# Performance work log

Measured on AMD Instinct MI355X. Metric: run time of the kernel, lower is better.

The kernel has to match this reference:

```python
import jax, jax.numpy as jnp
import numpy as np

B, S, H, F, E, TOP_K = 2, 1024, 2048, 1408, 8, 2
SHARED_F = 2 * F  # moe_intermediate_size * n_shared_experts


def setup_inputs() -> dict:
    key = jax.random.key(0)
    ks = jax.random.split(key, 8)
    s = 0.02  # init scale for weights
    return {
        "hidden_states": jax.random.normal(ks[0], (B, S, H), jnp.float32),
        "gate_weight": jax.random.normal(ks[1], (E, H), jnp.float32) * s,
        "gate_proj": jax.random.normal(ks[2], (E, H, F), jnp.float32) * s,
        "up_proj": jax.random.normal(ks[3], (E, H, F), jnp.float32) * s,
        "down_proj": jax.random.normal(ks[4], (E, F, H), jnp.float32) * s,
        "shared_gate": jax.random.normal(ks[5], (H, SHARED_F), jnp.float32) * s,
        "shared_up": jax.random.normal(ks[6], (H, SHARED_F), jnp.float32) * s,
        "shared_down": jax.random.normal(ks[7], (SHARED_F, H), jnp.float32) * s,
    }


def reference(hidden_states, gate_weight, gate_proj, up_proj, down_proj,
              shared_gate, shared_up, shared_down):
    orig_shape = hidden_states.shape
    x = hidden_states.reshape(-1, orig_shape[-1])  # [T, H]
    T = x.shape[0]

    # MoEGate: softmax scores, top-k routing (no renorm)
    scores = jax.nn.softmax(x @ gate_weight.T, axis=-1)  # [T, E]
    topk_w, topk_idx = jax.lax.top_k(scores, TOP_K)      # [T, K]
    # dense combine weights: zero except selected experts
    combine = jnp.zeros_like(scores).at[jnp.arange(T)[:, None], topk_idx].set(topk_w)  # [T, E]

    # FusedSigmaMLP on all experts (math equal to sort/pad/grouped-GEMM/scatter-add path)
    gate_h = jnp.einsum('td,edf->etf', x, gate_proj)     # [E, T, F]
    up_h = jnp.einsum('td,edf->etf', x, up_proj)          # [E, T, F]
    expert_out = jnp.einsum('etf,efd->etd', jax.nn.silu(gate_h) * up_h, down_proj)  # [E, T, H]
    y = jnp.einsum('etd,te->td', expert_out, combine)     # weighted combine

    # shared experts (SigmaMLP with intermediate = moe_intermediate * n_shared)
    shared = (jax.nn.silu(x @ shared_gate) * (x @ shared_up)) @ shared_down
    return (y + shared).reshape(orig_shape)
```

## Files before the change

kernel.cpp:

```cpp
#include <hip/hip_runtime.h>
#include <hip/hip_bf16.h>

constexpr int T_ = 2048;
constexpr int H_ = 2048;
constexpr int F_ = 1408;
constexpr int E_ = 8;
constexpr int SF_ = 2816;

typedef __bf16 bf16;
typedef bf16 bf16x4 __attribute__((ext_vector_type(4)));
typedef bf16 bf16x8 __attribute__((ext_vector_type(8)));
typedef float f32x4 __attribute__((ext_vector_type(4)));

#define DEVI __device__ __forceinline__

constexpr int TR_GRID = 5280;
constexpr int PREP_GRID = TR_GRID + T_;
constexpr int GU_SH = 768;
constexpr int GU_EX = 3072;
constexpr int GU_GRID = GU_SH + GU_EX;
constexpr int DNSH_GRID = 512;
constexpr int DNEX_GRID = 2048;

DEVI void async16(const void* g, void* l) {
    __builtin_amdgcn_global_load_lds(
        (const __attribute__((address_space(1))) unsigned int*)g,
        (__attribute__((address_space(3))) unsigned int*)l, 16, 0, 0);
}

DEVI void transpose_tile(const float* __restrict__ src, bf16* __restrict__ dst,
                         int R, int C, int t, bf16* tile ) {
    int tiles_c = C >> 7;
    int r0 = (t / tiles_c) * 128, c0 = (t % tiles_c) * 128;
    int th = threadIdx.x;
    int fr = th >> 5;
    int fc = (th & 31) * 4;
#pragma unroll
    for (int p = 0; p < 16; p++) {
        int r = fr + p * 8;
        float4 v = *(const float4*)(src + (size_t)(r0 + r) * C + c0 + fc);
        bf16x4 b;
        b[0] = (bf16)v.x; b[1] = (bf16)v.y; b[2] = (bf16)v.z; b[3] = (bf16)v.w;
        *(bf16x4*)(tile + r * 132 + (fc ^ (r & 0x7C))) = b;
    }
    __syncthreads();
#pragma unroll
    for (int p = 0; p < 8; p++) {
        int ch = p * 256 + th;
        int c = ch >> 4, rq = ch & 15;
        bf16x8 o;
#pragma unroll
        for (int j = 0; j < 8; j++) {
            int row = rq * 8 + j;
            o[j] = tile[row * 132 + (c ^ (row & 0x7C))];
        }
        *(bf16x8*)(dst + (size_t)(c0 + c) * R + r0 + rq * 8) = o;
    }
}

DEVI void gate_route_token(const float* __restrict__ x, const float* __restrict__ gw,
                           bf16* __restrict__ xb, int* __restrict__ cnt,
                           int* __restrict__ list, float* __restrict__ wlist,
                           int t, float* wred ) {
    int tid = threadIdx.x;
    const float* xr = x + (size_t)t * H_;
    int h0 = tid * 8;
    float4 a = *(const float4*)(xr + h0);
    float4 b = *(const float4*)(xr + h0 + 4);
    float xv[8] = {a.x, a.y, a.z, a.w, b.x, b.y, b.z, b.w};
    bf16x8 v;
#pragma unroll
    for (int j = 0; j < 8; j++) v[j] = (bf16)xv[j];
    *(bf16x8*)(xb + (size_t)t * H_ + h0) = v;

    float p[E_];
#pragma unroll
    for (int e = 0; e < E_; e++) p[e] = 0.f;
#pragma unroll
    for (int j = 0; j < 8; j++)
#pragma unroll
        for (int e = 0; e < E_; e++) p[e] += xv[j] * gw[e * H_ + h0 + j];
#pragma unroll
    for (int e = 0; e < E_; e++)
#pragma unroll
        for (int off = 32; off > 0; off >>= 1) p[e] += __shfl_down(p[e], off, 64);
    int lane = tid & 63, wid = tid >> 6;
    if (lane == 0)
#pragma unroll
        for (int e = 0; e < E_; e++) wred[wid * E_ + e] = p[e];
    __syncthreads();
    if (tid == 0) {
        float l[E_];
#pragma unroll
        for (int e = 0; e < E_; e++)
            l[e] = wred[0 * E_ + e] + wred[1 * E_ + e] + wred[2 * E_ + e] + wred[3 * E_ + e];
        float mx = l[0];
#pragma unroll
        for (int e = 1; e < E_; e++) mx = fmaxf(mx, l[e]);
        float sc[E_], s = 0.f;
#pragma unroll
        for (int e = 0; e < E_; e++) { sc[e] = __expf(l[e] - mx); s += sc[e]; }
#pragma unroll
        for (int e = 0; e < E_; e++) sc[e] /= s;
        int i1 = 0;
#pragma unroll
        for (int e = 1; e < E_; e++) if (sc[e] > sc[i1]) i1 = e;
        int i2 = (i1 == 0) ? 1 : 0;
#pragma unroll
        for (int e = 0; e < E_; e++) if (e != i1 && sc[e] > sc[i2]) i2 = e;
        int p1 = atomicAdd(&cnt[i1], 1);
        list[i1 * T_ + p1] = t; wlist[i1 * T_ + p1] = sc[i1];
        int p2 = atomicAdd(&cnt[i2], 1);
        list[i2 * T_ + p2] = t; wlist[i2 * T_ + p2] = sc[i2];
    }
}

__global__ void fused_prep(const float* __restrict__ gp, const float* __restrict__ up,
                           const float* __restrict__ dp, const float* __restrict__ sg,
                           const float* __restrict__ su, const float* __restrict__ sd,
                           bf16* __restrict__ wg, bf16* __restrict__ wu,
                           bf16* __restrict__ wd, bf16* __restrict__ sgt,
                           bf16* __restrict__ sut, bf16* __restrict__ sdt,
                           const float* __restrict__ x, const float* __restrict__ gw,
                           bf16* __restrict__ xb, int* __restrict__ cnt,
                           int* __restrict__ list, float* __restrict__ wlist) {
    __shared__ __align__(16) bf16 tile[128 * 132];
    int id = blockIdx.x;
    if (id >= TR_GRID) {
        gate_route_token(x, gw, xb, cnt, list, wlist, id - TR_GRID, (float*)tile);
        return;
    }
    const float* src; bf16* dst; int R, C, t;
    if (id < 1408)      { int e = id / 176; t = id % 176; R = 2048; C = 1408;
                          src = gp + (size_t)e * R * C; dst = wg + (size_t)e * R * C; }
    else if (id < 2816) { int e = (id - 1408) / 176; t = (id - 1408) % 176; R = 2048; C = 1408;
                          src = up + (size_t)e * R * C; dst = wu + (size_t)e * R * C; }
    else if (id < 4224) { int e = (id - 2816) / 176; t = (id - 2816) % 176; R = 1408; C = 2048;
                          src = dp + (size_t)e * R * C; dst = wd + (size_t)e * R * C; }
    else if (id < 4576) { t = id - 4224; R = 2048; C = 2816; src = sg; dst = sgt; }
    else if (id < 4928) { t = id - 4576; R = 2048; C = 2816; src = su; dst = sut; }
    else                { t = id - 4928; R = 2816; C = 2048; src = sd; dst = sdt; }
    transpose_tile(src, dst, R, C, t, tile);
}

__global__ void gemm_gu(const bf16* __restrict__ xb,
                        const bf16* __restrict__ sgt, const bf16* __restrict__ sut,
                        const bf16* __restrict__ wg, const bf16* __restrict__ wu,
                        bf16* __restrict__ act_sh, bf16* __restrict__ act,
                        const int* __restrict__ cnt, const int* __restrict__ list,
                        const float* __restrict__ wlist) {
    int id = blockIdx.x;
    const bf16 *Bg, *Bu; bf16* C;
    const float* wl = nullptr;
    const int* lstA = nullptr;
    int M, N, row0, col0;
    if (id < GU_SH) {
        int x = id & 7, u = id >> 3;
        int cg = u >> 4, rb = u & 15;
        int col = cg * 8 + x;
        if (col >= 44) return;
        Bg = sgt; Bu = sut; C = act_sh;
        M = T_; N = SF_; row0 = rb * 128; col0 = col * 64;
    } else {
        int id2 = id - GU_SH;
        int x = id2 & 7, u = id2 >> 3;
        int e = u / 48, t2 = u % 48, j = t2 >> 4, rb = t2 & 15;
        int col = ((x - e) & 7) + 8 * j;
        if (col >= 22) return;
        M = cnt[e]; row0 = rb * 128;
        if (row0 >= M) return;
        lstA = list + (size_t)e * T_;
        Bg = wg + (size_t)e * F_ * H_;
        Bu = wu + (size_t)e * F_ * H_;
        C = act + (size_t)e * T_ * F_;
        wl = wlist + (size_t)e * T_;
        N = F_; col0 = col * 64;
    }

    __shared__ __align__(16) bf16 As[128 * 64];
    __shared__ __align__(16) bf16 Bgs[64 * 64];
    __shared__ __align__(16) bf16 Bus[64 * 64];

    int tid = threadIdx.x, lane = tid & 63, wid = tid >> 6;
    int wm = (wid >> 1) * 64, wn = (wid & 1) * 32;
    int lm = lane & 15, lq = lane >> 4;

    int srcrow[4];
#pragma unroll
    for (int j = 0; j < 4; j++) {
        int m = (j * 256 + tid) >> 3;
        int gr = row0 + m; if (gr >= M) gr = M - 1;
        srcrow[j] = lstA ? lstA[gr] : gr;
    }

    f32x4 accg[4][2] = {};
    f32x4 accu[4][2] = {};
    constexpr int nkt = H_ >> 6;

    for (int kt = 0; kt < nkt; kt++) {
        int k0 = kt * 64;
#pragma unroll
        for (int j = 0; j < 4; j++) {
            int L = j * 256 + tid;
            int m = L >> 3, cp = L & 7, c = cp ^ (m & 7);
            async16(xb + (size_t)srcrow[j] * H_ + k0 + c * 8, (void*)(As + L * 8));
        }
#pragma unroll
        for (int j = 0; j < 2; j++) {
            int L = j * 256 + tid;
            int n = L >> 3, cp = L & 7, c = cp ^ (n & 7);
            async16(Bg + (size_t)(col0 + n) * H_ + k0 + c * 8, (void*)(Bgs + L * 8));
            async16(Bu + (size_t)(col0 + n) * H_ + k0 + c * 8, (void*)(Bus + L * 8));
        }
        __syncthreads();
#pragma unroll
        for (int kk = 0; kk < 2; kk++) {
            bf16x8 af[4], bgf[2], buf_[2];
            int cc = kk * 4 + lq;
#pragma unroll
            for (int mi = 0; mi < 4; mi++) {
                int r = wm + mi * 16 + lm;
                af[mi] = *(const bf16x8*)(As + r * 64 + ((cc ^ (r & 7)) * 8));
            }
#pragma unroll
            for (int ni = 0; ni < 2; ni++) {
                int r = wn + ni * 16 + lm;
                bgf[ni]  = *(const bf16x8*)(Bgs + r * 64 + ((cc ^ (r & 7)) * 8));
                buf_[ni] = *(const bf16x8*)(Bus + r * 64 + ((cc ^ (r & 7)) * 8));
            }
#pragma unroll
            for (int mi = 0; mi < 4; mi++)
#pragma unroll
                for (int ni = 0; ni < 2; ni++) {
                    accg[mi][ni] = __builtin_amdgcn_mfma_f32_16x16x32_bf16(af[mi], bgf[ni], accg[mi][ni], 0, 0, 0);
                    accu[mi][ni] = __builtin_amdgcn_mfma_f32_16x16x32_bf16(af[mi], buf_[ni], accu[mi][ni], 0, 0, 0);
                }
        }
        __syncthreads();
    }
#pragma unroll
    for (int mi = 0; mi < 4; mi++)
#pragma unroll
        for (int r = 0; r < 4; r++) {
            int gr = row0 + wm + mi * 16 + lq * 4 + r;
            if (gr >= M) continue;
            float wv = wl ? wl[gr] : 1.f;
#pragma unroll
            for (int ni = 0; ni < 2; ni++) {
                int gc = col0 + wn + ni * 16 + lm;
                float g = accg[mi][ni][r], u = accu[mi][ni][r];
                float actv = wv * (g / (1.f + __expf(-g)) * u);
                C[(size_t)gr * N + gc] = (bf16)actv;
            }
        }
}

__global__ void gemm_down_sh(const bf16* __restrict__ act_sh, const bf16* __restrict__ sdt,
                             float* __restrict__ out) {
    int id = blockIdx.x;
    int x = id & 7, u = id >> 3;
    int cg = u >> 4, rb = u & 15;
    int col = cg * 8 + x;
    int row0 = rb * 128, col0 = col * 64;

    __shared__ __align__(16) bf16 As[128 * 64];
    __shared__ __align__(16) bf16 Bs[64 * 64];

    int tid = threadIdx.x, lane = tid & 63, wid = tid >> 6;
    int wm = (wid >> 1) * 64, wn = (wid & 1) * 32;
    int lm = lane & 15, lq = lane >> 4;

    f32x4 acc[4][2] = {};
    constexpr int nkt = SF_ >> 6;

    for (int kt = 0; kt < nkt; kt++) {
        int k0 = kt * 64;
#pragma unroll
        for (int j = 0; j < 4; j++) {
            int L = j * 256 + tid;
            int m = L >> 3, cp = L & 7, c = cp ^ (m & 7);
            async16(act_sh + (size_t)(row0 + m) * SF_ + k0 + c * 8, (void*)(As + L * 8));
        }
#pragma unroll
        for (int j = 0; j < 2; j++) {
            int L = j * 256 + tid;
            int n = L >> 3, cp = L & 7, c = cp ^ (n & 7);
            async16(sdt + (size_t)(col0 + n) * SF_ + k0 + c * 8, (void*)(Bs + L * 8));
        }
        __syncthreads();
#pragma unroll
        for (int kk = 0; kk < 2; kk++) {
            bf16x8 af[4], bfr[2];
            int cc = kk * 4 + lq;
#pragma unroll
            for (int i = 0; i < 4; i++) {
                int r = wm + i * 16 + lm;
                af[i] = *(const bf16x8*)(As + r * 64 + ((cc ^ (r & 7)) * 8));
            }
#pragma unroll
            for (int ni = 0; ni < 2; ni++) {
                int r = wn + ni * 16 + lm;
                bfr[ni] = *(const bf16x8*)(Bs + r * 64 + ((cc ^ (r & 7)) * 8));
            }
#pragma unroll
            for (int mi = 0; mi < 4; mi++)
#pragma unroll
                for (int ni = 0; ni < 2; ni++)
                    acc[mi][ni] = __builtin_amdgcn_mfma_f32_16x16x32_bf16(af[mi], bfr[ni], acc[mi][ni], 0, 0, 0);
        }
        __syncthreads();
    }
#pragma unroll
    for (int mi = 0; mi < 4; mi++)
#pragma unroll
        for (int r = 0; r < 4; r++) {
            int t = row0 + wm + mi * 16 + lq * 4 + r;
#pragma unroll
            for (int ni = 0; ni < 2; ni++) {
                int gc = col0 + wn + ni * 16 + lm;
                out[(size_t)t * H_ + gc] = acc[mi][ni][r];
            }
        }
}

__global__ void gemm_down_ex(const bf16* __restrict__ act, const bf16* __restrict__ wd,
                             float* __restrict__ out, const int* __restrict__ cnt,
                             const int* __restrict__ list) {
    int id = blockIdx.x;
    int x = id & 7, u = id >> 3;
    int e = u >> 5, t2 = u & 31, j = t2 >> 4, rb = t2 & 15;
    int col = ((x - e) & 7) + 8 * j;
    int M = cnt[e], row0 = rb * 128;
    if (row0 >= M) return;
    const bf16* A = act + (size_t)e * T_ * F_;
    const bf16* B = wd + (size_t)e * H_ * F_;
    const int* lst = list + (size_t)e * T_;
    int col0 = col * 128;

    __shared__ __align__(16) bf16 As[128 * 64];
    __shared__ __align__(16) bf16 Bs[128 * 64];

    int tid = threadIdx.x, lane = tid & 63, wid = tid >> 6;
    int wm = (wid >> 1) * 64, wn = (wid & 1) * 64;
    int lm = lane & 15, lq = lane >> 4;

    f32x4 acc[4][4] = {};
    constexpr int nkt = F_ >> 6;

    for (int kt = 0; kt < nkt; kt++) {
        int k0 = kt * 64;
#pragma unroll
        for (int j2 = 0; j2 < 4; j2++) {
            int L = j2 * 256 + tid;
            int m = L >> 3, cp = L & 7, c = cp ^ (m & 7);
            int gr = row0 + m; if (gr >= M) gr = M - 1;
            async16(A + (size_t)gr * F_ + k0 + c * 8, (void*)(As + L * 8));
            async16(B + (size_t)(col0 + m) * F_ + k0 + c * 8, (void*)(Bs + L * 8));
        }
        __syncthreads();
#pragma unroll
        for (int kk = 0; kk < 2; kk++) {
            bf16x8 af[4], bfr[4];
            int cc = kk * 4 + lq;
#pragma unroll
            for (int i = 0; i < 4; i++) {
                int ra = wm + i * 16 + lm;
                af[i] = *(const bf16x8*)(As + ra * 64 + ((cc ^ (ra & 7)) * 8));
                int rb2 = wn + i * 16 + lm;
                bfr[i] = *(const bf16x8*)(Bs + rb2 * 64 + ((cc ^ (rb2 & 7)) * 8));
            }
#pragma unroll
            for (int mi = 0; mi < 4; mi++)
#pragma unroll
                for (int ni = 0; ni < 4; ni++)
                    acc[mi][ni] = __builtin_amdgcn_mfma_f32_16x16x32_bf16(af[mi], bfr[ni], acc[mi][ni], 0, 0, 0);
        }
        __syncthreads();
    }
#pragma unroll
    for (int mi = 0; mi < 4; mi++)
#pragma unroll
        for (int r = 0; r < 4; r++) {
            int cr = row0 + wm + mi * 16 + lq * 4 + r;
            if (cr >= M) continue;
            int t = lst[cr];
#pragma unroll
            for (int ni = 0; ni < 4; ni++) {
                int gc = col0 + wn + ni * 16 + lm;
                atomicAdd(&out[(size_t)t * H_ + gc], acc[mi][ni][r]);
            }
        }
}

extern "C" void kernel_launch(void* const* d_in, const int* in_sizes, int n_in,
                              void* d_out, int out_size, void* d_ws, size_t ws_size,
                              hipStream_t stream) {
    const float* x     = (const float*)d_in[0];
    const float* gw    = (const float*)d_in[1];
    const float* gproj = (const float*)d_in[2];
    const float* uproj = (const float*)d_in[3];
    const float* dproj = (const float*)d_in[4];
    const float* sg    = (const float*)d_in[5];
    const float* su    = (const float*)d_in[6];
    const float* sd    = (const float*)d_in[7];
    float* out = (float*)d_out;

    char* w = (char*)d_ws;
    size_t off = 0;
    auto alloc = [&](size_t bytes) { void* p = w + off; off += (bytes + 255) & ~(size_t)255; return p; };
    bf16* wg_t   = (bf16*)alloc((size_t)E_ * F_ * H_ * 2);
    bf16* wu_t   = (bf16*)alloc((size_t)E_ * F_ * H_ * 2);
    bf16* wd_t   = (bf16*)alloc((size_t)E_ * H_ * F_ * 2);
    bf16* sg_t   = (bf16*)alloc((size_t)SF_ * H_ * 2);
    bf16* su_t   = (bf16*)alloc((size_t)SF_ * H_ * 2);
    bf16* sd_t   = (bf16*)alloc((size_t)H_ * SF_ * 2);
    bf16* xb     = (bf16*)alloc((size_t)T_ * H_ * 2);
    bf16* act    = (bf16*)alloc((size_t)E_ * T_ * F_ * 2);
    bf16* act_sh = (bf16*)alloc((size_t)T_ * SF_ * 2);
    int*  cnt    = (int*)alloc(256);
    int*  list   = (int*)alloc((size_t)E_ * T_ * 4);
    float* wlist = (float*)alloc((size_t)E_ * T_ * 4);
    (void)ws_size; (void)in_sizes; (void)n_in; (void)out_size;

    hipMemsetAsync(cnt, 0, 256, stream);

    fused_prep<<<PREP_GRID, 256, 0, stream>>>(gproj, uproj, dproj, sg, su, sd,
                                              wg_t, wu_t, wd_t, sg_t, su_t, sd_t,
                                              x, gw, xb, cnt, list, wlist);

    gemm_gu<<<GU_GRID, 256, 0, stream>>>(xb, sg_t, su_t, wg_t, wu_t,
                                         act_sh, act, cnt, list, wlist);
    gemm_down_sh<<<DNSH_GRID, 256, 0, stream>>>(act_sh, sd_t, out);
    gemm_down_ex<<<DNEX_GRID, 256, 0, stream>>>(act, wd_t, out, cnt, list);
}
```

Baseline: 598.4 us.

## Move down-projection weight transposes into gate/up GEMM launch to overlap

The down-projection weight transposes (expert and shared) move out of the prep kernel and into extra blocks appended to the gate/up GEMM grid, so that conversion runs alongside the GEMM blocks instead of ahead of them. The GEMM's shared memory becomes one union buffer sized for the transpose tile (about 33KB versus 32KB), which could slightly reduce occupancy. The transpose load loop is also restructured to issue four float4 loads before converting, to raise memory-level parallelism. The transpose blocks come last in the grid and may run as a tail after the GEMM blocks.

Result: no change. 591.8 us (-1.1%).

```diff
diff --git a/kernel.cpp b/kernel.cpp
--- a/kernel.cpp
+++ b/kernel.cpp
@@ -14,11 +14,13 @@
 
 #define DEVI __device__ __forceinline__
 
-constexpr int TR_GRID = 5280;
-constexpr int PREP_GRID = TR_GRID + T_;
+constexpr int TR_PREP = 3520;
+constexpr int PREP_GRID = TR_PREP + T_;
 constexpr int GU_SH = 768;
 constexpr int GU_EX = 3072;
 constexpr int GU_GRID = GU_SH + GU_EX;
+constexpr int TR_GU = 1760;
+constexpr int GU_GRID_TOT = GU_GRID + TR_GU;
 constexpr int DNSH_GRID = 512;
 constexpr int DNEX_GRID = 2048;
 
@@ -36,11 +38,24 @@
     int fr = th >> 5;
     int fc = (th & 31) * 4;
 #pragma unroll
-    for (int p = 0; p < 16; p++) {
-        int r = fr + p * 8;
-        float4 v = *(const float4*)(src + (size_t)(r0 + r) * C + c0 + fc);
+    for (int p4 = 0; p4 < 4; p4++) {
+        float4 v0 = *(const float4*)(src + (size_t)(r0 + fr + (p4 * 4 + 0) * 8) * C + c0 + fc);
+        float4 v1 = *(const float4*)(src + (size_t)(r0 + fr + (p4 * 4 + 1) * 8) * C + c0 + fc);
+        float4 v2 = *(const float4*)(src + (size_t)(r0 + fr + (p4 * 4 + 2) * 8) * C + c0 + fc);
+        float4 v3 = *(const float4*)(src + (size_t)(r0 + fr + (p4 * 4 + 3) * 8) * C + c0 + fc);
+        int r;
         bf16x4 b;
-        b[0] = (bf16)v.x; b[1] = (bf16)v.y; b[2] = (bf16)v.z; b[3] = (bf16)v.w;
+        r = fr + (p4 * 4 + 0) * 8;
+        b[0] = (bf16)v0.x; b[1] = (bf16)v0.y; b[2] = (bf16)v0.z; b[3] = (bf16)v0.w;
+        *(bf16x4*)(tile + r * 132 + (fc ^ (r & 0x7C))) = b;
+        r = fr + (p4 * 4 + 1) * 8;
+        b[0] = (bf16)v1.x; b[1] = (bf16)v1.y; b[2] = (bf16)v1.z; b[3] = (bf16)v1.w;
+        *(bf16x4*)(tile + r * 132 + (fc ^ (r & 0x7C))) = b;
+        r = fr + (p4 * 4 + 2) * 8;
+        b[0] = (bf16)v2.x; b[1] = (bf16)v2.y; b[2] = (bf16)v2.z; b[3] = (bf16)v2.w;
+        *(bf16x4*)(tile + r * 132 + (fc ^ (r & 0x7C))) = b;
+        r = fr + (p4 * 4 + 3) * 8;
+        b[0] = (bf16)v3.x; b[1] = (bf16)v3.y; b[2] = (bf16)v3.z; b[3] = (bf16)v3.w;
         *(bf16x4*)(tile + r * 132 + (fc ^ (r & 0x7C))) = b;
     }
     __syncthreads();
@@ -116,18 +131,16 @@
 }
 
 __global__ void fused_prep(const float* __restrict__ gp, const float* __restrict__ up,
-                           const float* __restrict__ dp, const float* __restrict__ sg,
-                           const float* __restrict__ su, const float* __restrict__ sd,
+                           const float* __restrict__ sg, const float* __restrict__ su,
                            bf16* __restrict__ wg, bf16* __restrict__ wu,
-                           bf16* __restrict__ wd, bf16* __restrict__ sgt,
-                           bf16* __restrict__ sut, bf16* __restrict__ sdt,
+                           bf16* __restrict__ sgt, bf16* __restrict__ sut,
                            const float* __restrict__ x, const float* __restrict__ gw,
                            bf16* __restrict__ xb, int* __restrict__ cnt,
                            int* __restrict__ list, float* __restrict__ wlist) {
     __shared__ __align__(16) bf16 tile[128 * 132];
     int id = blockIdx.x;
-    if (id >= TR_GRID) {
-        gate_route_token(x, gw, xb, cnt, list, wlist, id - TR_GRID, (float*)tile);
+    if (id >= TR_PREP) {
+        gate_route_token(x, gw, xb, cnt, list, wlist, id - TR_PREP, (float*)tile);
         return;
     }
     const float* src; bf16* dst; int R, C, t;
@@ -135,11 +148,8 @@
                           src = gp + (size_t)e * R * C; dst = wg + (size_t)e * R * C; }
     else if (id < 2816) { int e = (id - 1408) / 176; t = (id - 1408) % 176; R = 2048; C = 1408;
                           src = up + (size_t)e * R * C; dst = wu + (size_t)e * R * C; }
-    else if (id < 4224) { int e = (id - 2816) / 176; t = (id - 2816) % 176; R = 1408; C = 2048;
-                          src = dp + (size_t)e * R * C; dst = wd + (size_t)e * R * C; }
-    else if (id < 4576) { t = id - 4224; R = 2048; C = 2816; src = sg; dst = sgt; }
-    else if (id < 4928) { t = id - 4576; R = 2048; C = 2816; src = su; dst = sut; }
-    else                { t = id - 4928; R = 2816; C = 2048; src = sd; dst = sdt; }
+    else if (id < 3168) { t = id - 2816; R = 2048; C = 2816; src = sg; dst = sgt; }
+    else                { t = id - 3168; R = 2048; C = 2816; src = su; dst = sut; }
     transpose_tile(src, dst, R, C, t, tile);
 }
 
@@ -148,8 +158,24 @@
                         const bf16* __restrict__ wg, const bf16* __restrict__ wu,
                         bf16* __restrict__ act_sh, bf16* __restrict__ act,
                         const int* __restrict__ cnt, const int* __restrict__ list,
-                        const float* __restrict__ wlist) {
+                        const float* __restrict__ wlist,
+                        const float* __restrict__ dp, const float* __restrict__ sd,
+                        bf16* __restrict__ wd, bf16* __restrict__ sdt) {
+    __shared__ __align__(16) bf16 smem[128 * 132];
     int id = blockIdx.x;
+    if (id >= GU_GRID) {
+        int id2 = id - GU_GRID;
+        const float* src; bf16* dst; int R, C, t;
+        if (id2 < 1408) { int e = id2 / 176; t = id2 % 176; R = 1408; C = 2048;
+                          src = dp + (size_t)e * R * C; dst = wd + (size_t)e * R * C; }
+        else            { t = id2 - 1408; R = 2816; C = 2048; src = sd; dst = sdt; }
+        transpose_tile(src, dst, R, C, t, smem);
+        return;
+    }
+    bf16* As  = smem;
+    bf16* Bgs = smem + 128 * 64;
+    bf16* Bus = smem + 128 * 64 + 64 * 64;
+
     const bf16 *Bg, *Bu; bf16* C;
     const float* wl = nullptr;
     const int* lstA = nullptr;
@@ -177,10 +203,6 @@
         N = F_; col0 = col * 64;
     }
 
-    __shared__ __align__(16) bf16 As[128 * 64];
-    __shared__ __align__(16) bf16 Bgs[64 * 64];
-    __shared__ __align__(16) bf16 Bus[64 * 64];
-
     int tid = threadIdx.x, lane = tid & 63, wid = tid >> 6;
     int wm = (wid >> 1) * 64, wn = (wid & 1) * 32;
     int lm = lane & 15, lq = lane >> 4;
@@ -424,12 +446,13 @@
 
     hipMemsetAsync(cnt, 0, 256, stream);
 
-    fused_prep<<<PREP_GRID, 256, 0, stream>>>(gproj, uproj, dproj, sg, su, sd,
-                                              wg_t, wu_t, wd_t, sg_t, su_t, sd_t,
+    fused_prep<<<PREP_GRID, 256, 0, stream>>>(gproj, uproj, sg, su,
+                                              wg_t, wu_t, sg_t, su_t,
                                               x, gw, xb, cnt, list, wlist);
 
-    gemm_gu<<<GU_GRID, 256, 0, stream>>>(xb, sg_t, su_t, wg_t, wu_t,
-                                         act_sh, act, cnt, list, wlist);
+    gemm_gu<<<GU_GRID_TOT, 256, 0, stream>>>(xb, sg_t, su_t, wg_t, wu_t,
+                                             act_sh, act, cnt, list, wlist,
+                                             dproj, sd, wd_t, sd_t);
     gemm_down_sh<<<DNSH_GRID, 256, 0, stream>>>(act_sh, sd_t, out);
     gemm_down_ex<<<DNEX_GRID, 256, 0, stream>>>(act, wd_t, out, cnt, list);
 }
```
